# Kernel optimization log

Hardware: AMD Instinct MI355X
Metric: run time of the kernel (lower is better)

Reference implementation:

```python
import jax, jax.numpy as jnp
import numpy as np

B, L, H, N, O = 64, 512, 768, 50, 768
ALPHA = 0.3  # leaky relu slope in GAT
NEG_INF = -9e15


def _position_encoding(n, d):
    # standard sinusoidal PE, shape [n, d]
    pos = jnp.arange(n, dtype=jnp.float32)[:, None]              # [n,1]
    div = jnp.exp(jnp.arange(0, d, 2, dtype=jnp.float32) * (-np.log(10000.0) / d))  # [d/2]
    ang = pos * div[None, :]                                     # [n, d/2]
    return jnp.stack([jnp.sin(ang), jnp.cos(ang)], axis=-1).reshape(n, d)


def _gat_layer(x, adj, W, b, a, ab):
    # Dense GAT layer. Original builds an [N,N,2F] concat tensor then applies
    # linear a; mathematically identical to splitting a into src/dst halves.
    Wh = x @ W + b                                               # [N,F]
    Fdim = Wh.shape[-1]
    a_src = Wh @ a[:Fdim]                                        # [N]
    a_dst = Wh @ a[Fdim:]                                        # [N]
    e = jax.nn.leaky_relu(a_src[:, None] + a_dst[None, :] + ab, negative_slope=ALPHA)
    att = jax.nn.softmax(jnp.where(adj > 0, e, NEG_INF), axis=1)  # rows sum to 1
    return att @ Wh                                              # [N,F]


def setup_inputs() -> dict:
    key = jax.random.key(0)
    ks = jax.random.split(key, 16)
    s = 1.0 / np.sqrt(H)
    utter_embedding = jax.random.normal(ks[0], (B, L, H), jnp.float32)
    cls_ids = jnp.sort(jax.random.randint(ks[1], (B, N), 0, L), axis=1).astype(jnp.int32)
    adj = jax.random.randint(ks[2], (B, N, N), 0, 2).astype(jnp.int32)
    adj = adj | jnp.eye(N, dtype=jnp.int32)  # ensure self loops so softmax rows are valid
    return {
        "utter_embedding": utter_embedding,
        "cls_ids": cls_ids,
        "adj": adj,
        # GAT head 0 (concat=True)
        "W1": jax.random.normal(ks[3], (H, H), jnp.float32) * s,
        "b1": jnp.zeros((H,), jnp.float32),
        "a1": jax.random.normal(ks[4], (2 * H,), jnp.float32) * s,
        "ab1": jnp.zeros((), jnp.float32),
        # GAT out layer (concat=False)
        "W2": jax.random.normal(ks[5], (H, H), jnp.float32) * s,
        "b2": jnp.zeros((H,), jnp.float32),
        "a2": jax.random.normal(ks[6], (2 * H,), jnp.float32) * s,
        "ab2": jnp.zeros((), jnp.float32),
        # Attention pooling over utterances
        "Wa": jax.random.normal(ks[7], (H, H), jnp.float32) * s,
        "ba": jnp.zeros((H,), jnp.float32),
        "v": jax.random.normal(ks[8], (H,), jnp.float32) * s,
        # Final linear
        "Wl": jax.random.normal(ks[9], (H, O), jnp.float32) * s,
        "bl": jnp.zeros((O,), jnp.float32),
    }


def reference(utter_embedding, cls_ids, adj, W1, b1, a1, ab1, W2, b2, a2, ab2,
              Wa, ba, v, Wl, bl):
    pe = _position_encoding(N, H)                                # [N,H]

    def per_dialogue(emb, ids, A):
        # gather [CLS] utterance embeddings: index_select
        x = jnp.take(emb, ids, axis=0)                           # [N,H]
        x = x + pe                                               # position encoder
        # GAT: 1 head concat -> elu, out layer -> elu, residual
        h = jax.nn.elu(_gat_layer(x, A, W1, b1, a1, ab1))
        h = jax.nn.elu(_gat_layer(h, A, W2, b2, a2, ab2)) + x    # residual per GAT.forward
        # attention pooling over N utterances
        scores = jax.nn.softmax(jnp.tanh(h @ Wa + ba) @ v, axis=0)  # [N]
        return scores @ h                                        # [H]

    dialogue = jax.vmap(per_dialogue)(utter_embedding, cls_ids, adj)  # [B,H]
    return dialogue @ Wl + bl                                    # [B,O]
```

## Files before the change

kernel.cpp:

```cpp
#include <hip/hip_runtime.h>
#include <hip/hip_bf16.h>
#include <math.h>

typedef __attribute__((ext_vector_type(8))) short bf16x8;
typedef __attribute__((ext_vector_type(4))) float f32x4;

constexpr int Bn = 64;
constexpr int Ln = 512;
constexpr int Hd = 768;
constexpr int Nn = 50;
constexpr int On = 768;

struct PrepArgs {
  const float* src[4];
  __hip_bfloat16* dst[4];
  const float* emb;
  const int* ids;
  float* xf;
  __hip_bfloat16* xb;
  float* aux;
  int auxn;
};

__global__ __launch_bounds__(256) void prep_kernel(PrepArgs a) {
  __shared__ float tile[32][33];
  int bx = blockIdx.x;
  if (bx < 2304) {
    int job = bx / 576, t = bx % 576;
    const float* W = a.src[job];
    __hip_bfloat16* Wt = a.dst[job];
    int tx = (t % 24) * 32, ty = (t / 24) * 32;
    int c = threadIdx.x & 31, r0 = threadIdx.x >> 5;
    for (int r = r0; r < 32; r += 8)
      tile[r][c] = W[(size_t)(tx + r) * Hd + ty + c];
    __syncthreads();
    for (int r = r0; r < 32; r += 8)
      Wt[(size_t)(ty + r) * Hd + tx + c] = __float2bfloat16(tile[c][r]);
  } else if (bx < 5504) {
    int bn = bx - 2304;
    int b = bn / Nn, n = bn % Nn;
    int id = a.ids[bn];
    const float* src = a.emb + ((size_t)b * Ln + id) * Hd;
    float* xo = a.xf + (size_t)bn * Hd;
    __hip_bfloat16* xbo = a.xb + (size_t)bn * Hd;
    const float kLog = 9.210340371976184f / (float)Hd;
    for (int h = threadIdx.x; h < Hd; h += 256) {
      int he = h & ~1;
      float freq = expf(-(float)he * kLog);
      float ang = (float)n * freq;
      float pe = (h & 1) ? cosf(ang) : sinf(ang);
      float v = src[h] + pe;
      xo[h] = v;
      xbo[h] = __float2bfloat16(v);
    }
  } else {
    int idx = (bx - 5504) * 256 + threadIdx.x;
    if (idx < a.auxn) a.aux[idx] = 0.f;
  }
}

template <int EPI>
__global__ __launch_bounds__(256) void gemm_kernel(
    const __hip_bfloat16* __restrict__ A, const __hip_bfloat16* __restrict__ Bt,
    const float* __restrict__ bias, __hip_bfloat16* __restrict__ C,
    const float* __restrict__ avec, float* __restrict__ o1,
    float* __restrict__ o2) {
  __shared__ __hip_bfloat16 As[2][64][40];
  __shared__ __hip_bfloat16 Bs[2][64][40];
  int tid = threadIdx.x;
  int wave = tid >> 6, lane = tid & 63;
  int lr = lane & 15, lq = lane >> 4;
  int row0 = blockIdx.x * 64, col0 = blockIdx.y * 64;
  int sr = tid >> 2, sk = (tid & 3) * 8;
  const __hip_bfloat16* Ap = A + (size_t)(row0 + sr) * Hd + sk;
  const __hip_bfloat16* Bp = Bt + (size_t)(col0 + sr) * Hd + sk;
  uint4 ra = *(const uint4*)Ap;
  uint4 rb = *(const uint4*)Bp;
  *(uint4*)&As[0][sr][sk] = ra;
  *(uint4*)&Bs[0][sr][sk] = rb;
  f32x4 acc[4] = {};
  __syncthreads();
  int cur = 0;
  for (int kt = 32; kt < Hd; kt += 32) {
    ra = *(const uint4*)(Ap + kt);
    rb = *(const uint4*)(Bp + kt);
    bf16x8 af = *(const bf16x8*)&As[cur][wave * 16 + lr][lq * 8];
#pragma unroll
    for (int ct = 0; ct < 4; ++ct) {
      bf16x8 bfrag = *(const bf16x8*)&Bs[cur][ct * 16 + lr][lq * 8];
      acc[ct] = __builtin_amdgcn_mfma_f32_16x16x32_bf16(af, bfrag, acc[ct], 0, 0, 0);
    }
    *(uint4*)&As[cur ^ 1][sr][sk] = ra;
    *(uint4*)&Bs[cur ^ 1][sr][sk] = rb;
    __syncthreads();
    cur ^= 1;
  }
  {
    bf16x8 af = *(const bf16x8*)&As[cur][wave * 16 + lr][lq * 8];
#pragma unroll
    for (int ct = 0; ct < 4; ++ct) {
      bf16x8 bfrag = *(const bf16x8*)&Bs[cur][ct * 16 + lr][lq * 8];
      acc[ct] = __builtin_amdgcn_mfma_f32_16x16x32_bf16(af, bfrag, acc[ct], 0, 0, 0);
    }
  }
  int cr0 = row0 + wave * 16 + lq * 4;
  if (EPI == 0) {
    float ps[4] = {}, pd[4] = {};
#pragma unroll
    for (int ct = 0; ct < 4; ++ct) {
      int gc = col0 + ct * 16 + lr;
      float bv = bias[gc];
      float as_ = avec[gc], ad_ = avec[Hd + gc];
#pragma unroll
      for (int r = 0; r < 4; ++r) {
        float v = acc[ct][r] + bv;
        C[(size_t)(cr0 + r) * Hd + gc] = __float2bfloat16(v);
        ps[r] += v * as_;
        pd[r] += v * ad_;
      }
    }
#pragma unroll
    for (int off = 8; off; off >>= 1)
#pragma unroll
      for (int r = 0; r < 4; ++r) {
        ps[r] += __shfl_xor(ps[r], off);
        pd[r] += __shfl_xor(pd[r], off);
      }
    if (lr == 0)
#pragma unroll
      for (int r = 0; r < 4; ++r) {
        atomicAdd(&o1[cr0 + r], ps[r]);
        atomicAdd(&o2[cr0 + r], pd[r]);
      }
  } else {
    float pr[4] = {};
#pragma unroll
    for (int ct = 0; ct < 4; ++ct) {
      int gc = col0 + ct * 16 + lr;
      float bv = bias[gc];
      float vv_ = avec[gc];
#pragma unroll
      for (int r = 0; r < 4; ++r) {
        float t = tanhf(acc[ct][r] + bv);
        pr[r] += t * vv_;
      }
    }
#pragma unroll
    for (int off = 8; off; off >>= 1)
#pragma unroll
      for (int r = 0; r < 4; ++r) pr[r] += __shfl_xor(pr[r], off);
    if (lr == 0)
#pragma unroll
      for (int r = 0; r < 4; ++r) atomicAdd(&o1[cr0 + r], pr[r]);
  }
}

template <int LAYER>
__global__ __launch_bounds__(256) void attf_kernel(
    const float* __restrict__ ssrc, const float* __restrict__ sdst,
    const int* __restrict__ adj, const float* __restrict__ ab,
    const __hip_bfloat16* __restrict__ Wh, const float* __restrict__ xres,
    float* __restrict__ hf, __hip_bfloat16* __restrict__ hb) {
  int b = blockIdx.x / 6, h0 = (blockIdx.x % 6) * 128;
  __shared__ float attL[Nn * Nn];
  float abv = ab[0];
  for (int idx = threadIdx.x; idx < Nn * Nn; idx += 256) {
    int i = idx / Nn, j = idx - i * Nn;
    float t = ssrc[b * Nn + i] + sdst[b * Nn + j] + abv;
    t = t > 0.f ? t : 0.3f * t;
    attL[idx] = (adj[(size_t)b * Nn * Nn + idx] > 0) ? t : -9.0e15f;
  }
  __syncthreads();
  if (threadIdx.x < Nn) {
    int i = threadIdx.x;
    float m = -3.0e38f;
    for (int j = 0; j < Nn; ++j) m = fmaxf(m, attL[i * Nn + j]);
    float s = 0.f;
    for (int j = 0; j < Nn; ++j) {
      float p = expf(attL[i * Nn + j] - m);
      attL[i * Nn + j] = p;
      s += p;
    }
    float inv = 1.f / s;
    for (int j = 0; j < Nn; ++j) attL[i * Nn + j] *= inv;
  }
  __syncthreads();
  int col = threadIdx.x & 127, half = threadIdx.x >> 7;
  int i0 = half * 25;
  float acc[25] = {};
  const __hip_bfloat16* Whb = Wh + ((size_t)b * Nn) * Hd + h0 + col;
  for (int j = 0; j < Nn; j += 2) {
    float w0 = __bfloat162float(Whb[(size_t)j * Hd]);
    float w1 = __bfloat162float(Whb[(size_t)(j + 1) * Hd]);
#pragma unroll
    for (int ii = 0; ii < 25; ++ii) {
      float2 a2 = *(const float2*)&attL[(i0 + ii) * Nn + j];
      acc[ii] += a2.x * w0 + a2.y * w1;
    }
  }
#pragma unroll
  for (int ii = 0; ii < 25; ++ii) {
    float v = acc[ii];
    v = v > 0.f ? v : expf(v) - 1.f;
    size_t off = ((size_t)b * Nn + i0 + ii) * Hd + h0 + col;
    if (LAYER == 2) {
      v += xres[off];
      hf[off] = v;
    }
    hb[off] = __float2bfloat16(v);
  }
}

__global__ __launch_bounds__(256) void poolfinal_kernel(
    const float* __restrict__ sraw, const float* __restrict__ h2,
    const __hip_bfloat16* __restrict__ Wlt, const float* __restrict__ bl,
    float* __restrict__ out) {
  int b = blockIdx.x;
  __shared__ float sc[Nn];
  __shared__ float ds[Hd];
  if (threadIdx.x < 64) {
    int j = threadIdx.x;
    float e = (j < Nn) ? sraw[b * Nn + j] : -3.0e38f;
    float m = e;
#pragma unroll
    for (int off = 32; off; off >>= 1) m = fmaxf(m, __shfl_xor(m, off));
    float p = (j < Nn) ? expf(e - m) : 0.f;
    float s = p;
#pragma unroll
    for (int off = 32; off; off >>= 1) s += __shfl_xor(s, off);
    if (j < Nn) sc[j] = p / s;
  }
  __syncthreads();
  for (int h = threadIdx.x; h < Hd; h += 256) {
    float a = 0.f;
#pragma unroll 10
    for (int j = 0; j < Nn; ++j) a += sc[j] * h2[((size_t)b * Nn + j) * Hd + h];
    ds[h] = a;
  }
  __syncthreads();
  for (int oo = 0; oo < 3; ++oo) {
    int o = oo * 256 + threadIdx.x;
    float acc = bl[o];
    const uint4* wr = (const uint4*)(Wlt + (size_t)o * Hd);
    for (int kk = 0; kk < Hd / 8; ++kk) {
      union { uint4 u; unsigned short s[8]; } w;
      w.u = wr[kk];
#pragma unroll
      for (int t = 0; t < 8; ++t)
        acc += ds[kk * 8 + t] * __uint_as_float((unsigned)w.s[t] << 16);
    }
    out[(size_t)b * On + o] = acc;
  }
}

extern "C" void kernel_launch(void* const* d_in, const int* in_sizes, int n_in,
                              void* d_out, int out_size, void* d_ws, size_t ws_size,
                              hipStream_t stream) {
  const float* emb = (const float*)d_in[0];
  const int* ids = (const int*)d_in[1];
  const int* adj = (const int*)d_in[2];
  const float* W1 = (const float*)d_in[3];
  const float* b1 = (const float*)d_in[4];
  const float* a1 = (const float*)d_in[5];
  const float* ab1 = (const float*)d_in[6];
  const float* W2 = (const float*)d_in[7];
  const float* b2 = (const float*)d_in[8];
  const float* a2 = (const float*)d_in[9];
  const float* ab2 = (const float*)d_in[10];
  const float* Wa = (const float*)d_in[11];
  const float* ba = (const float*)d_in[12];
  const float* vv = (const float*)d_in[13];
  const float* Wl = (const float*)d_in[14];
  const float* bl = (const float*)d_in[15];
  float* out = (float*)d_out;

  char* p = (char*)d_ws;
  auto alloc = [&](size_t bytes) {
    char* r = p;
    p += (bytes + 255) & ~(size_t)255;
    return r;
  };
  __hip_bfloat16* Wt1 = (__hip_bfloat16*)alloc((size_t)Hd * Hd * 2);
  __hip_bfloat16* Wt2 = (__hip_bfloat16*)alloc((size_t)Hd * Hd * 2);
  __hip_bfloat16* Wta = (__hip_bfloat16*)alloc((size_t)Hd * Hd * 2);
  __hip_bfloat16* Wlt = (__hip_bfloat16*)alloc((size_t)Hd * On * 2);
  float* aux = (float*)alloc(5 * Bn * Nn * 4);
  float* ssrc1 = aux;
  float* sdst1 = aux + Bn * Nn;
  float* ssrc2 = aux + 2 * Bn * Nn;
  float* sdst2 = aux + 3 * Bn * Nn;
  float* sraw = aux + 4 * Bn * Nn;
  float* xf = (float*)alloc((size_t)Bn * Nn * Hd * 4);
  __hip_bfloat16* xb = (__hip_bfloat16*)alloc((size_t)Bn * Nn * Hd * 2);
  __hip_bfloat16* Whb16 = (__hip_bfloat16*)alloc((size_t)Bn * Nn * Hd * 2);
  float* h2f = (float*)alloc((size_t)Bn * Nn * Hd * 4);
  __hip_bfloat16* hb = (__hip_bfloat16*)alloc((size_t)Bn * Nn * Hd * 2);

  PrepArgs pa;
  pa.src[0] = W1; pa.src[1] = W2; pa.src[2] = Wa; pa.src[3] = Wl;
  pa.dst[0] = Wt1; pa.dst[1] = Wt2; pa.dst[2] = Wta; pa.dst[3] = Wlt;
  pa.emb = emb; pa.ids = ids; pa.xf = xf; pa.xb = xb;
  pa.aux = aux; pa.auxn = 5 * Bn * Nn;
  prep_kernel<<<5567, 256, 0, stream>>>(pa);

  dim3 ggrid(Bn * Nn / 64, Hd / 64);
  dim3 agrid(6 * Bn);

  gemm_kernel<0><<<ggrid, 256, 0, stream>>>(xb, Wt1, b1, Whb16, a1, ssrc1,
                                            sdst1);
  attf_kernel<1><<<agrid, 256, 0, stream>>>(ssrc1, sdst1, adj, ab1, Whb16,
                                            nullptr, nullptr, hb);
  gemm_kernel<0><<<ggrid, 256, 0, stream>>>(hb, Wt2, b2, Whb16, a2, ssrc2,
                                            sdst2);
  attf_kernel<2><<<agrid, 256, 0, stream>>>(ssrc2, sdst2, adj, ab2, Whb16, xf,
                                            h2f, hb);
  gemm_kernel<1><<<ggrid, 256, 0, stream>>>(hb, Wta, ba, nullptr, vv, sraw,
                                            nullptr);
  poolfinal_kernel<<<Bn, 256, 0, stream>>>(sraw, h2f, Wlt, bl, out);
}
```

Before: 305.8 us.

## Pad dialogues to 64 rows and use MFMA for attention aggregation

Each dialogue's 50 nodes are padded to 64 rows so a GEMM tile maps to exactly one dialogue. The first GEMM's output is written transposed (per dialogue, feature-major) so the attention-times-Wh product can run on bf16 MFMA instead of scalar FP32 loops. This replaces the scalar 50x50x768 aggregation with tensor-core work and halves the attention grid. In exchange it does about 28% more GEMM work on padding rows, and it rounds attention weights to bf16, which reduces precision.

```diff
diff --git a/kernel.cpp b/kernel.cpp
--- a/kernel.cpp
+++ b/kernel.cpp
@@ -4,28 +4,37 @@
 
 typedef __attribute__((ext_vector_type(8))) short bf16x8;
 typedef __attribute__((ext_vector_type(4))) float f32x4;
+typedef __attribute__((ext_vector_type(4))) unsigned short u16x4;
 
 constexpr int Bn = 64;
 constexpr int Ln = 512;
 constexpr int Hd = 768;
 constexpr int Nn = 50;
 constexpr int On = 768;
+constexpr int RP = 64;
+
+__device__ __forceinline__ f32x4 MFMA(bf16x8 a, bf16x8 b, f32x4 c) {
+  return __builtin_amdgcn_mfma_f32_16x16x32_bf16(a, b, c, 0, 0, 0);
+}
+__device__ __forceinline__ unsigned short f2bb(float v) {
+  __hip_bfloat16 h = __float2bfloat16(v);
+  return *(unsigned short*)&h;
+}
 
 struct PrepArgs {
   const float* src[4];
   __hip_bfloat16* dst[4];
   const float* emb;
   const int* ids;
-  float* xf;
+  float* xres;
   __hip_bfloat16* xb;
   float* aux;
-  int auxn;
 };
 
 __global__ __launch_bounds__(256) void prep_kernel(PrepArgs a) {
-  __shared__ float tile[32][33];
   int bx = blockIdx.x;
   if (bx < 2304) {
+    __shared__ float tile[32][33];
     int job = bx / 576, t = bx % 576;
     const float* W = a.src[job];
     __hip_bfloat16* Wt = a.dst[job];
@@ -36,33 +45,38 @@
     __syncthreads();
     for (int r = r0; r < 32; r += 8)
       Wt[(size_t)(ty + r) * Hd + tx + c] = __float2bfloat16(tile[c][r]);
-  } else if (bx < 5504) {
+  } else if (bx < 6400) {
     int bn = bx - 2304;
-    int b = bn / Nn, n = bn % Nn;
-    int id = a.ids[bn];
-    const float* src = a.emb + ((size_t)b * Ln + id) * Hd;
-    float* xo = a.xf + (size_t)bn * Hd;
+    int b = bn >> 6, i = bn & 63;
     __hip_bfloat16* xbo = a.xb + (size_t)bn * Hd;
-    const float kLog = 9.210340371976184f / (float)Hd;
-    for (int h = threadIdx.x; h < Hd; h += 256) {
-      int he = h & ~1;
-      float freq = expf(-(float)he * kLog);
-      float ang = (float)n * freq;
-      float pe = (h & 1) ? cosf(ang) : sinf(ang);
-      float v = src[h] + pe;
-      xo[h] = v;
-      xbo[h] = __float2bfloat16(v);
+    float* xro = a.xres + (size_t)bn * Hd;
+    if (i < Nn) {
+      int id = a.ids[b * Nn + i];
+      const float* src = a.emb + ((size_t)b * Ln + id) * Hd;
+      const float kLog = 9.210340371976184f / (float)Hd;
+      for (int h = threadIdx.x; h < Hd; h += 256) {
+        float freq = expf(-(float)(h & ~1) * kLog);
+        float ang = (float)i * freq;
+        float v = src[h] + ((h & 1) ? cosf(ang) : sinf(ang));
+        xbo[h] = __float2bfloat16(v);
+        xro[h] = v;
+      }
+    } else {
+      for (int h = threadIdx.x; h < Hd; h += 256) {
+        xbo[h] = __float2bfloat16(0.f);
+        xro[h] = 0.f;
+      }
     }
   } else {
-    int idx = (bx - 5504) * 256 + threadIdx.x;
-    if (idx < a.auxn) a.aux[idx] = 0.f;
+    int idx = (bx - 6400) * 256 + threadIdx.x;
+    if (idx < 5 * Bn * RP) a.aux[idx] = 0.f;
   }
 }
 
 template <int EPI>
 __global__ __launch_bounds__(256) void gemm_kernel(
     const __hip_bfloat16* __restrict__ A, const __hip_bfloat16* __restrict__ Bt,
-    const float* __restrict__ bias, __hip_bfloat16* __restrict__ C,
+    const float* __restrict__ bias, __hip_bfloat16* __restrict__ WhT,
     const float* __restrict__ avec, float* __restrict__ o1,
     float* __restrict__ o2) {
   __shared__ __hip_bfloat16 As[2][64][40];
@@ -70,7 +84,8 @@
   int tid = threadIdx.x;
   int wave = tid >> 6, lane = tid & 63;
   int lr = lane & 15, lq = lane >> 4;
-  int row0 = blockIdx.x * 64, col0 = blockIdx.y * 64;
+  int b = blockIdx.x, col0 = blockIdx.y * 64;
+  int row0 = b * RP;
   int sr = tid >> 2, sk = (tid & 3) * 8;
   const __hip_bfloat16* Ap = A + (size_t)(row0 + sr) * Hd + sk;
   const __hip_bfloat16* Bp = Bt + (size_t)(col0 + sr) * Hd + sk;
@@ -86,10 +101,8 @@
     rb = *(const uint4*)(Bp + kt);
     bf16x8 af = *(const bf16x8*)&As[cur][wave * 16 + lr][lq * 8];
 #pragma unroll
-    for (int ct = 0; ct < 4; ++ct) {
-      bf16x8 bfrag = *(const bf16x8*)&Bs[cur][ct * 16 + lr][lq * 8];
-      acc[ct] = __builtin_amdgcn_mfma_f32_16x16x32_bf16(af, bfrag, acc[ct], 0, 0, 0);
-    }
+    for (int ct = 0; ct < 4; ++ct)
+      acc[ct] = MFMA(af, *(const bf16x8*)&Bs[cur][ct * 16 + lr][lq * 8], acc[ct]);
     *(uint4*)&As[cur ^ 1][sr][sk] = ra;
     *(uint4*)&Bs[cur ^ 1][sr][sk] = rb;
     __syncthreads();
@@ -98,26 +111,26 @@
   {
     bf16x8 af = *(const bf16x8*)&As[cur][wave * 16 + lr][lq * 8];
 #pragma unroll
-    for (int ct = 0; ct < 4; ++ct) {
-      bf16x8 bfrag = *(const bf16x8*)&Bs[cur][ct * 16 + lr][lq * 8];
-      acc[ct] = __builtin_amdgcn_mfma_f32_16x16x32_bf16(af, bfrag, acc[ct], 0, 0, 0);
-    }
-  }
-  int cr0 = row0 + wave * 16 + lq * 4;
+    for (int ct = 0; ct < 4; ++ct)
+      acc[ct] = MFMA(af, *(const bf16x8*)&Bs[cur][ct * 16 + lr][lq * 8], acc[ct]);
+  }
+  int lrow0 = wave * 16 + lq * 4;
   if (EPI == 0) {
     float ps[4] = {}, pd[4] = {};
 #pragma unroll
     for (int ct = 0; ct < 4; ++ct) {
       int gc = col0 + ct * 16 + lr;
       float bv = bias[gc];
-      float as_ = avec[gc], ad_ = avec[Hd + gc];
+      float a_s = avec[gc], a_d = avec[Hd + gc];
+      u16x4 pk;
 #pragma unroll
       for (int r = 0; r < 4; ++r) {
         float v = acc[ct][r] + bv;
-        C[(size_t)(cr0 + r) * Hd + gc] = __float2bfloat16(v);
-        ps[r] += v * as_;
-        pd[r] += v * ad_;
-      }
+        pk[r] = f2bb(v);
+        ps[r] += v * a_s;
+        pd[r] += v * a_d;
+      }
+      *(u16x4*)(WhT + ((size_t)b * Hd + gc) * RP + lrow0) = pk;
     }
 #pragma unroll
     for (int off = 8; off; off >>= 1)
@@ -129,8 +142,11 @@
     if (lr == 0)
 #pragma unroll
       for (int r = 0; r < 4; ++r) {
-        atomicAdd(&o1[cr0 + r], ps[r]);
-        atomicAdd(&o2[cr0 + r], pd[r]);
+        int row = lrow0 + r;
+        if (row < Nn) {
+          atomicAdd(&o1[b * RP + row], ps[r]);
+          atomicAdd(&o2[b * RP + row], pd[r]);
+        }
       }
   } else {
     float pr[4] = {};
@@ -140,10 +156,7 @@
       float bv = bias[gc];
       float vv_ = avec[gc];
 #pragma unroll
-      for (int r = 0; r < 4; ++r) {
-        float t = tanhf(acc[ct][r] + bv);
-        pr[r] += t * vv_;
-      }
+      for (int r = 0; r < 4; ++r) pr[r] += tanhf(acc[ct][r] + bv) * vv_;
     }
 #pragma unroll
     for (int off = 8; off; off >>= 1)
@@ -151,7 +164,10 @@
       for (int r = 0; r < 4; ++r) pr[r] += __shfl_xor(pr[r], off);
     if (lr == 0)
 #pragma unroll
-      for (int r = 0; r < 4; ++r) atomicAdd(&o1[cr0 + r], pr[r]);
+      for (int r = 0; r < 4; ++r) {
+        int row = lrow0 + r;
+        if (row < Nn) atomicAdd(&o1[b * RP + row], pr[r]);
+      }
   }
 }
 
@@ -159,55 +175,61 @@
 __global__ __launch_bounds__(256) void attf_kernel(
     const float* __restrict__ ssrc, const float* __restrict__ sdst,
     const int* __restrict__ adj, const float* __restrict__ ab,
-    const __hip_bfloat16* __restrict__ Wh, const float* __restrict__ xres,
+    const __hip_bfloat16* __restrict__ WhT, const float* __restrict__ xres,
     float* __restrict__ hf, __hip_bfloat16* __restrict__ hb) {
-  int b = blockIdx.x / 6, h0 = (blockIdx.x % 6) * 128;
-  __shared__ float attL[Nn * Nn];
+  int b = blockIdx.x / 3, cg = blockIdx.x % 3;
+  __shared__ float attL[Nn * 52];
+  __shared__ __hip_bfloat16 attB[64 * 72];
+  int tid = threadIdx.x;
   float abv = ab[0];
-  for (int idx = threadIdx.x; idx < Nn * Nn; idx += 256) {
+  for (int i = tid; i < 64 * 72; i += 256) attB[i] = __float2bfloat16(0.f);
+  for (int idx = tid; idx < Nn * Nn; idx += 256) {
     int i = idx / Nn, j = idx - i * Nn;
-    float t = ssrc[b * Nn + i] + sdst[b * Nn + j] + abv;
+    float t = ssrc[b * RP + i] + sdst[b * RP + j] + abv;
     t = t > 0.f ? t : 0.3f * t;
-    attL[idx] = (adj[(size_t)b * Nn * Nn + idx] > 0) ? t : -9.0e15f;
-  }
-  __syncthreads();
-  if (threadIdx.x < Nn) {
-    int i = threadIdx.x;
+    attL[i * 52 + j] = (adj[(size_t)b * Nn * Nn + idx] > 0) ? t : -9.0e15f;
+  }
+  __syncthreads();
+  if (tid < Nn) {
     float m = -3.0e38f;
-    for (int j = 0; j < Nn; ++j) m = fmaxf(m, attL[i * Nn + j]);
+    for (int j = 0; j < Nn; ++j) m = fmaxf(m, attL[tid * 52 + j]);
     float s = 0.f;
     for (int j = 0; j < Nn; ++j) {
-      float p = expf(attL[i * Nn + j] - m);
-      attL[i * Nn + j] = p;
+      float p = expf(attL[tid * 52 + j] - m);
+      attL[tid * 52 + j] = p;
       s += p;
     }
     float inv = 1.f / s;
-    for (int j = 0; j < Nn; ++j) attL[i * Nn + j] *= inv;
-  }
-  __syncthreads();
-  int col = threadIdx.x & 127, half = threadIdx.x >> 7;
-  int i0 = half * 25;
-  float acc[25] = {};
-  const __hip_bfloat16* Whb = Wh + ((size_t)b * Nn) * Hd + h0 + col;
-  for (int j = 0; j < Nn; j += 2) {
-    float w0 = __bfloat162float(Whb[(size_t)j * Hd]);
-    float w1 = __bfloat162float(Whb[(size_t)(j + 1) * Hd]);
-#pragma unroll
-    for (int ii = 0; ii < 25; ++ii) {
-      float2 a2 = *(const float2*)&attL[(i0 + ii) * Nn + j];
-      acc[ii] += a2.x * w0 + a2.y * w1;
-    }
-  }
-#pragma unroll
-  for (int ii = 0; ii < 25; ++ii) {
-    float v = acc[ii];
-    v = v > 0.f ? v : expf(v) - 1.f;
-    size_t off = ((size_t)b * Nn + i0 + ii) * Hd + h0 + col;
-    if (LAYER == 2) {
-      v += xres[off];
-      hf[off] = v;
-    }
-    hb[off] = __float2bfloat16(v);
+    for (int j = 0; j < Nn; ++j) attL[tid * 52 + j] *= inv;
+  }
+  __syncthreads();
+  for (int idx = tid; idx < Nn * Nn; idx += 256) {
+    int i = idx / Nn, j = idx - i * Nn;
+    attB[i * 72 + j] = __float2bfloat16(attL[i * 52 + j]);
+  }
+  __syncthreads();
+
+  int w = tid >> 6, lane = tid & 63, lr = lane & 15, lq = lane >> 4;
+  bf16x8 a0 = *(const bf16x8*)&attB[(w * 16 + lr) * 72 + lq * 8];
+  bf16x8 a1 = *(const bf16x8*)&attB[(w * 16 + lr) * 72 + 32 + lq * 8];
+#pragma unroll
+  for (int s = 0; s < 16; ++s) {
+    int gc = cg * 256 + s * 16 + lr;
+    const __hip_bfloat16* Bp = WhT + ((size_t)b * Hd + gc) * RP + lq * 8;
+    f32x4 acc = {};
+    acc = MFMA(a0, *(const bf16x8*)Bp, acc);
+    acc = MFMA(a1, *(const bf16x8*)(Bp + 32), acc);
+#pragma unroll
+    for (int r = 0; r < 4; ++r) {
+      float v = acc[r];
+      v = v > 0.f ? v : expf(v) - 1.f;
+      size_t off = ((size_t)b * RP + w * 16 + lq * 4 + r) * Hd + gc;
+      if (LAYER == 2) {
+        v += xres[off];
+        hf[off] = v;
+      }
+      hb[off] = __float2bfloat16(v);
+    }
   }
 }
 
@@ -220,7 +242,7 @@
   __shared__ float ds[Hd];
   if (threadIdx.x < 64) {
     int j = threadIdx.x;
-    float e = (j < Nn) ? sraw[b * Nn + j] : -3.0e38f;
+    float e = (j < Nn) ? sraw[b * RP + j] : -3.0e38f;
     float m = e;
 #pragma unroll
     for (int off = 32; off; off >>= 1) m = fmaxf(m, __shfl_xor(m, off));
@@ -234,7 +256,7 @@
   for (int h = threadIdx.x; h < Hd; h += 256) {
     float a = 0.f;
 #pragma unroll 10
-    for (int j = 0; j < Nn; ++j) a += sc[j] * h2[((size_t)b * Nn + j) * Hd + h];
+    for (int j = 0; j < Nn; ++j) a += sc[j] * h2[((size_t)b * RP + j) * Hd + h];
     ds[h] = a;
   }
   __syncthreads();
@@ -284,37 +306,36 @@
   __hip_bfloat16* Wt2 = (__hip_bfloat16*)alloc((size_t)Hd * Hd * 2);
   __hip_bfloat16* Wta = (__hip_bfloat16*)alloc((size_t)Hd * Hd * 2);
   __hip_bfloat16* Wlt = (__hip_bfloat16*)alloc((size_t)Hd * On * 2);
-  float* aux = (float*)alloc(5 * Bn * Nn * 4);
+  float* aux = (float*)alloc((size_t)5 * Bn * RP * 4);
   float* ssrc1 = aux;
-  float* sdst1 = aux + Bn * Nn;
-  float* ssrc2 = aux + 2 * Bn * Nn;
-  float* sdst2 = aux + 3 * Bn * Nn;
-  float* sraw = aux + 4 * Bn * Nn;
-  float* xf = (float*)alloc((size_t)Bn * Nn * Hd * 4);
-  __hip_bfloat16* xb = (__hip_bfloat16*)alloc((size_t)Bn * Nn * Hd * 2);
-  __hip_bfloat16* Whb16 = (__hip_bfloat16*)alloc((size_t)Bn * Nn * Hd * 2);
-  float* h2f = (float*)alloc((size_t)Bn * Nn * Hd * 4);
-  __hip_bfloat16* hb = (__hip_bfloat16*)alloc((size_t)Bn * Nn * Hd * 2);
+  float* sdst1 = aux + Bn * RP;
+  float* ssrc2 = aux + 2 * Bn * RP;
+  float* sdst2 = aux + 3 * Bn * RP;
+  float* sraw = aux + 4 * Bn * RP;
+  __hip_bfloat16* xb = (__hip_bfloat16*)alloc((size_t)Bn * RP * Hd * 2);
+  float* xres = (float*)alloc((size_t)Bn * RP * Hd * 4);
+  __hip_bfloat16* WhT1 = (__hip_bfloat16*)alloc((size_t)Bn * Hd * RP * 2);
+  __hip_bfloat16* WhT2 = (__hip_bfloat16*)alloc((size_t)Bn * Hd * RP * 2);
+  __hip_bfloat16* h1b = (__hip_bfloat16*)alloc((size_t)Bn * RP * Hd * 2);
+  __hip_bfloat16* h2b = (__hip_bfloat16*)alloc((size_t)Bn * RP * Hd * 2);
+  float* h2f = (float*)alloc((size_t)Bn * RP * Hd * 4);
 
   PrepArgs pa;
   pa.src[0] = W1; pa.src[1] = W2; pa.src[2] = Wa; pa.src[3] = Wl;
   pa.dst[0] = Wt1; pa.dst[1] = Wt2; pa.dst[2] = Wta; pa.dst[3] = Wlt;
-  pa.emb = emb; pa.ids = ids; pa.xf = xf; pa.xb = xb;
-  pa.aux = aux; pa.auxn = 5 * Bn * Nn;
-  prep_kernel<<<5567, 256, 0, stream>>>(pa);
-
-  dim3 ggrid(Bn * Nn / 64, Hd / 64);
-  dim3 agrid(6 * Bn);
-
-  gemm_kernel<0><<<ggrid, 256, 0, stream>>>(xb, Wt1, b1, Whb16, a1, ssrc1,
-                                            sdst1);
-  attf_kernel<1><<<agrid, 256, 0, stream>>>(ssrc1, sdst1, adj, ab1, Whb16,
-                                            nullptr, nullptr, hb);
-  gemm_kernel<0><<<ggrid, 256, 0, stream>>>(hb, Wt2, b2, Whb16, a2, ssrc2,
-                                            sdst2);
-  attf_kernel<2><<<agrid, 256, 0, stream>>>(ssrc2, sdst2, adj, ab2, Whb16, xf,
-                                            h2f, hb);
-  gemm_kernel<1><<<ggrid, 256, 0, stream>>>(hb, Wta, ba, nullptr, vv, sraw,
+  pa.emb = emb; pa.ids = ids; pa.xres = xres; pa.xb = xb; pa.aux = aux;
+  prep_kernel<<<6480, 256, 0, stream>>>(pa);
+
+  dim3 ggrid(Bn, Hd / 64);
+  dim3 agrid(Bn * 3);
+
+  gemm_kernel<0><<<ggrid, 256, 0, stream>>>(xb, Wt1, b1, WhT1, a1, ssrc1, sdst1);
+  attf_kernel<1><<<agrid, 256, 0, stream>>>(ssrc1, sdst1, adj, ab1, WhT1,
+                                            nullptr, nullptr, h1b);
+  gemm_kernel<0><<<ggrid, 256, 0, stream>>>(h1b, Wt2, b2, WhT2, a2, ssrc2, sdst2);
+  attf_kernel<2><<<agrid, 256, 0, stream>>>(ssrc2, sdst2, adj, ab2, WhT2, xres,
+                                            h2f, h2b);
+  gemm_kernel<1><<<ggrid, 256, 0, stream>>>(h2b, Wta, ba, nullptr, vv, sraw,
                                             nullptr);
   poolfinal_kernel<<<Bn, 256, 0, stream>>>(sraw, h2f, Wlt, bl, out);
 }
```

New measurement: 305.5 us. Within noise of the previous version (-0.1%).
